# Performance work log

Hardware: AMD Instinct MI355X
Metric: run time of the kernel (lower is better)

Reference implementation:

```python
import jax, jax.numpy as jnp
import numpy as np

B, S, H = 2, 4096, 256
NH, NKV = 8, 4
HD = H // NH          # 32
GROUPS = NH // NKV    # 2
ROPE_BASE = 10000.0


def _rope_cos_sin(seq_len, dim, dtype):
    inv_freq = 1.0 / (ROPE_BASE ** (jnp.arange(0, dim, 2, dtype=jnp.float32) / dim))
    t = jnp.arange(seq_len, dtype=jnp.float32)
    freqs = jnp.outer(t, inv_freq)            # [S, dim/2]
    emb = jnp.concatenate([freqs, freqs], -1)  # [S, dim]
    return jnp.cos(emb).astype(dtype), jnp.sin(emb).astype(dtype)


def _rotate_half(x):
    x1, x2 = jnp.split(x, 2, axis=-1)
    return jnp.concatenate([-x2, x1], axis=-1)


def setup_inputs() -> dict:
    key = jax.random.key(0)
    k0, k1, k2, k3, k4 = jax.random.split(key, 5)
    return {
        "hidden_states": jax.random.normal(k0, (B, S, H), jnp.float32),
        "Wq": jax.random.normal(k1, (H, H), jnp.float32) * 0.02,
        "Wk": jax.random.normal(k2, (NKV * HD, H), jnp.float32) * 0.02,
        "Wv": jax.random.normal(k3, (NKV * HD, H), jnp.float32) * 0.02,
        "Wo": jax.random.normal(k4, (H, H), jnp.float32) * 0.02,
    }


def reference(hidden_states, Wq, Wk, Wv, Wo):
    b, s, _ = hidden_states.shape
    # projections (nn.Linear: x @ W.T)
    q = (hidden_states @ Wq.T).reshape(b, s, NH, HD).transpose(0, 2, 1, 3)   # [b,nh,s,hd]
    k = (hidden_states @ Wk.T).reshape(b, s, NKV, HD).transpose(0, 2, 1, 3)  # [b,nkv,s,hd]
    v = (hidden_states @ Wv.T).reshape(b, s, NKV, HD).transpose(0, 2, 1, 3)
    # RoPE
    cos, sin = _rope_cos_sin(s, HD, hidden_states.dtype)  # [s,hd]
    q = q * cos + _rotate_half(q) * sin
    k = k * cos + _rotate_half(k) * sin
    # GQA: repeat kv heads (repeat_interleave over head dim)
    k = jnp.repeat(k, GROUPS, axis=1)  # [b,nh,s,hd]
    v = jnp.repeat(v, GROUPS, axis=1)
    # scores + causal mask
    scores = jnp.einsum('bhqd,bhkd->bhqk', q, k) / jnp.sqrt(jnp.float32(HD)).astype(q.dtype)
    causal = jnp.triu(jnp.full((s, s), -jnp.inf, dtype=scores.dtype), k=1)
    scores = scores + causal
    attn = jax.nn.softmax(scores.astype(jnp.float32), axis=-1).astype(q.dtype)
    out = jnp.einsum('bhqk,bhkd->bhqd', attn, v)          # [b,nh,s,hd]
    out = out.transpose(0, 2, 1, 3).reshape(b, s, NH * HD)
    return out @ Wo.T
```

## Files before the change

kernel.cpp:

```cpp
#include <hip/hip_runtime.h>
#include <hip/hip_bf16.h>
#include <stdint.h>

#define NB 2
#define SEQ 4096
#define HID 256
#define NHEAD 8
#define NKVH 4
#define HDIM 32

typedef __bf16 bf16;
typedef __bf16 bf16x8 __attribute__((ext_vector_type(8)));
typedef float f32x4 __attribute__((ext_vector_type(4)));

static __device__ __forceinline__ uint16_t bfbits(float f) {
    bf16 h = (bf16)f;
    return __builtin_bit_cast(uint16_t, h);
}
static __device__ __forceinline__ uint32_t pack_bf16(float lo, float hi) {
    return (uint32_t)bfbits(lo) | ((uint32_t)bfbits(hi) << 16);
}
static __device__ __forceinline__ float fexp2(float x) {
#if __has_builtin(__builtin_amdgcn_exp2f)
    return __builtin_amdgcn_exp2f(x);
#else
    float r; asm("v_exp_f32 %0, %1" : "=v"(r) : "v"(x)); return r;
#endif
}
static __device__ __forceinline__ void gld_lds16(const void* g, void* l) {
    __builtin_amdgcn_global_load_lds(
        (const __attribute__((address_space(1))) void*)g,
        (__attribute__((address_space(3))) void*)l, 16, 0, 0);
}

__global__ __launch_bounds__(256) void qkv_proj(
    const float* __restrict__ hs, const float* __restrict__ Wq,
    const float* __restrict__ Wk, const float* __restrict__ Wv,
    bf16* __restrict__ qws, bf16* __restrict__ kws, bf16* __restrict__ vtws)
{
    __shared__ bf16 As[64][136];
    __shared__ bf16 Bs[64][136];
    const int t = threadIdx.x;
    const int wid = t >> 6, lane = t & 63;
    const int g = lane >> 4, c = lane & 15;
    const int n0 = blockIdx.x * 64;
    const int m0 = blockIdx.y * 64;

    const float* bsrc; int ro;
    if (n0 < 256)      { bsrc = Wq; ro = n0; }
    else if (n0 < 384) { bsrc = Wk; ro = n0 - 256; }
    else               { bsrc = Wv; ro = n0 - 384; }

    const f32x4 zf = {0.f, 0.f, 0.f, 0.f};
    f32x4 acc[4] = {zf, zf, zf, zf};

    const int c4 = t & 31;
    const int rb = t >> 5;

    for (int ks = 0; ks < 256; ks += 128) {
        __syncthreads();
        #pragma unroll
        for (int i = 0; i < 8; ++i) {
            int row = i * 8 + rb;
            float4 v = *(const float4*)&hs[(size_t)(m0 + row) * HID + ks + c4 * 4];
            ushort4 w; w.x = bfbits(v.x); w.y = bfbits(v.y); w.z = bfbits(v.z); w.w = bfbits(v.w);
            *(ushort4*)&As[row][c4 * 4] = w;
        }
        #pragma unroll
        for (int i = 0; i < 8; ++i) {
            int row = i * 8 + rb;
            float4 v = *(const float4*)&bsrc[(size_t)(ro + row) * HID + ks + c4 * 4];
            ushort4 w; w.x = bfbits(v.x); w.y = bfbits(v.y); w.z = bfbits(v.z); w.w = bfbits(v.w);
            *(ushort4*)&Bs[row][c4 * 4] = w;
        }
        __syncthreads();
        #pragma unroll
        for (int kk = 0; kk < 128; kk += 32) {
            bf16x8 af = *(const bf16x8*)&As[wid * 16 + c][kk + g * 8];
            #pragma unroll
            for (int nt = 0; nt < 4; ++nt) {
                bf16x8 bfr = *(const bf16x8*)&Bs[nt * 16 + c][kk + g * 8];
                acc[nt] = __builtin_amdgcn_mfma_f32_16x16x32_bf16(af, bfr, acc[nt], 0, 0, 0);
            }
        }
    }

    const float qscale = 1.4426950408889634f * 0.17677669529663687f;
    const float invf = exp2f(-0.83048202372184f * (float)c);
    #pragma unroll
    for (int r = 0; r < 4; ++r) {
        int m = m0 + wid * 16 + g * 4 + r;
        int b = m >> 12, s = m & (SEQ - 1);
        float sn, cs;
        sincosf((float)s * invf, &sn, &cs);
        if (n0 < 256) {
            #pragma unroll
            for (int np = 0; np < 4; np += 2) {
                int h = (n0 + np * 16) >> 5;
                float x1 = acc[np][r], x2 = acc[np + 1][r];
                float y1 = (x1 * cs - x2 * sn) * qscale;
                float y2 = (x2 * cs + x1 * sn) * qscale;
                size_t base = ((size_t)(b * NHEAD + h) * SEQ + s) * HDIM;
                qws[base + c] = (bf16)y1;
                qws[base + 16 + c] = (bf16)y2;
            }
        } else if (n0 < 384) {
            #pragma unroll
            for (int np = 0; np < 4; np += 2) {
                int kh = (n0 - 256 + np * 16) >> 5;
                float x1 = acc[np][r], x2 = acc[np + 1][r];
                float y1 = x1 * cs - x2 * sn;
                float y2 = x2 * cs + x1 * sn;
                size_t base = ((size_t)(b * NKVH + kh) * SEQ + s) * HDIM;
                kws[base + c] = (bf16)y1;
                kws[base + 16 + c] = (bf16)y2;
            }
        } else {
            #pragma unroll
            for (int nt = 0; nt < 4; ++nt) {
                int ng = n0 + nt * 16 + c - 384;
                int vh = ng >> 5, d = ng & 31;
                vtws[((size_t)(b * NKVH + vh) * HDIM + d) * SEQ + s] = (bf16)acc[nt][r];
            }
        }
    }
}

__global__ __launch_bounds__(256, 2) void attn_fwd(
    const bf16* __restrict__ qws, const bf16* __restrict__ kws,
    const bf16* __restrict__ vtws, bf16* __restrict__ att)
{
    __shared__ bf16 Kb[2][128 * 32];
    __shared__ bf16 Vb[2][32 * 128];
    __shared__ float tr[4][16 * 33];
    const int t = threadIdx.x;
    const int w = t >> 6, lane = t & 63;
    const int g = lane >> 4, c = lane & 15;
    const int wg = blockIdx.x;
    const int h = wg & 7;
    const int rem = (wg >> 3) & 31;
    const int b = rem & 1;
    const int tp = rem >> 1;
    const int T = (wg < 256) ? (31 - tp) : tp;
    const int kvh = h >> 1;
    const bf16* Kg = kws + (size_t)(b * NKVH + kvh) * SEQ * HDIM;
    const bf16* Vg = vtws + (size_t)(b * NKVH + kvh) * HDIM * SEQ;
    const int nsteps = T + 1;
    const int q0 = T * 128 + w * 32;

    const bf16* Qb = qws + (size_t)(b * NHEAD + h) * SEQ * HDIM;
    bf16x8 qf0 = *(const bf16x8*)&Qb[(size_t)(q0 + c) * HDIM + g * 8];
    bf16x8 qf1 = *(const bf16x8*)&Qb[(size_t)(q0 + 16 + c) * HDIM + g * 8];

    const bf16* kg_t = Kg + t * 8;
    const int seg_s = (t & 8) | ((t & 7) ^ ((t >> 4) & 7));
    const bf16* vg_tA = Vg + (size_t)(t >> 4) * SEQ + seg_s * 8;
    const bf16* vg_tB = vg_tA + (size_t)16 * SEQ;
    char* kl = (char*)&Kb[0][0] + w * 1024;
    char* vl = (char*)&Vb[0][0] + w * 1024;

    const int kperm = 8 * (c >> 2) + (c & 3);
    const int kro = kperm * 64 + g * 16;
    const int cx = c & 7;
    const int vrow0 = c * 256;
    const int voff0 = ((g) ^ cx) << 4;
    const int voff1 = ((4 + g) ^ cx) << 4;
    const int voff2 = 128 + voff0;
    const int voff3 = 128 + voff1;

    const f32x4 zf = {0.f, 0.f, 0.f, 0.f};
    union { uint32_t u[4]; bf16x8 v; } onesf;
    onesf.u[0] = onesf.u[1] = onesf.u[2] = onesf.u[3] = 0x3F803F80u;

    f32x4 o00 = zf, o01 = zf, ol0 = zf;
    f32x4 o10 = zf, o11 = zf, ol1 = zf;

    gld_lds16(kg_t, kl);
    gld_lds16(kg_t + 2048, kl + 4096);
    gld_lds16(vg_tA, vl);
    gld_lds16(vg_tB, vl + 4096);
    __syncthreads();

    #pragma unroll 1
    for (int s = 0; s < nsteps; ++s) {
        const int sn = s + 1;
        if (sn < nsteps) {
            const int bo = (sn & 1) * 8192;
            gld_lds16(kg_t + (size_t)sn * 4096, kl + bo);
            gld_lds16(kg_t + (size_t)sn * 4096 + 2048, kl + bo + 4096);
            gld_lds16(vg_tA + (size_t)sn * 128, vl + bo);
            gld_lds16(vg_tB + (size_t)sn * 128, vl + bo + 4096);
        }
        const char* kbuf = (const char*)&Kb[s & 1][0];
        const char* vbuf = (const char*)&Vb[s & 1][0];
        const bool diag = (s == T);
        const int qo0 = w * 32 + c;
        #pragma unroll
        for (int j = 0; j < 4; ++j) {
            if (diag && j > w) continue;
            const int voffj = (j == 0) ? voff0 : (j == 1) ? voff1 : (j == 2) ? voff2 : voff3;
            bf16x8 kf0 = *(const bf16x8*)(kbuf + j * 2048 + kro);
            bf16x8 kf1 = *(const bf16x8*)(kbuf + j * 2048 + kro + 256);
            bf16x8 vfA = *(const bf16x8*)(vbuf + vrow0 + voffj);
            bf16x8 vfB = *(const bf16x8*)(vbuf + 4096 + vrow0 + voffj);
            {
                f32x4 st0 = __builtin_amdgcn_mfma_f32_16x16x32_bf16(kf0, qf0, zf, 0, 0, 0);
                f32x4 st1 = __builtin_amdgcn_mfma_f32_16x16x32_bf16(kf1, qf0, zf, 0, 0, 0);
                if (diag) {
                    #pragma unroll
                    for (int r = 0; r < 4; ++r) {
                        if (j * 32 + 8 * g + r > qo0)     st0[r] = -1e30f;
                        if (j * 32 + 8 * g + 4 + r > qo0) st1[r] = -1e30f;
                    }
                }
                float p0 = fexp2(st0[0]), p1 = fexp2(st0[1]), p2 = fexp2(st0[2]), p3 = fexp2(st0[3]);
                float p4 = fexp2(st1[0]), p5 = fexp2(st1[1]), p6 = fexp2(st1[2]), p7 = fexp2(st1[3]);
                union { uint32_t u[4]; bf16x8 v; } pb;
                asm("v_cvt_pk_bf16_f32 %0, %1, %2" : "=v"(pb.u[0]) : "v"(p0), "v"(p1));
                asm("v_cvt_pk_bf16_f32 %0, %1, %2" : "=v"(pb.u[1]) : "v"(p2), "v"(p3));
                asm("v_cvt_pk_bf16_f32 %0, %1, %2" : "=v"(pb.u[2]) : "v"(p4), "v"(p5));
                asm("v_cvt_pk_bf16_f32 %0, %1, %2" : "=v"(pb.u[3]) : "v"(p6), "v"(p7));
                o00 = __builtin_amdgcn_mfma_f32_16x16x32_bf16(vfA, pb.v, o00, 0, 0, 0);
                o01 = __builtin_amdgcn_mfma_f32_16x16x32_bf16(vfB, pb.v, o01, 0, 0, 0);
                ol0 = __builtin_amdgcn_mfma_f32_16x16x32_bf16(onesf.v, pb.v, ol0, 0, 0, 0);
            }
            {
                f32x4 st0 = __builtin_amdgcn_mfma_f32_16x16x32_bf16(kf0, qf1, zf, 0, 0, 0);
                f32x4 st1 = __builtin_amdgcn_mfma_f32_16x16x32_bf16(kf1, qf1, zf, 0, 0, 0);
                if (diag) {
                    const int qo1 = qo0 + 16;
                    #pragma unroll
                    for (int r = 0; r < 4; ++r) {
                        if (j * 32 + 8 * g + r > qo1)     st0[r] = -1e30f;
                        if (j * 32 + 8 * g + 4 + r > qo1) st1[r] = -1e30f;
                    }
                }
                float p0 = fexp2(st0[0]), p1 = fexp2(st0[1]), p2 = fexp2(st0[2]), p3 = fexp2(st0[3]);
                float p4 = fexp2(st1[0]), p5 = fexp2(st1[1]), p6 = fexp2(st1[2]), p7 = fexp2(st1[3]);
                union { uint32_t u[4]; bf16x8 v; } pb;
                asm("v_cvt_pk_bf16_f32 %0, %1, %2" : "=v"(pb.u[0]) : "v"(p0), "v"(p1));
                asm("v_cvt_pk_bf16_f32 %0, %1, %2" : "=v"(pb.u[1]) : "v"(p2), "v"(p3));
                asm("v_cvt_pk_bf16_f32 %0, %1, %2" : "=v"(pb.u[2]) : "v"(p4), "v"(p5));
                asm("v_cvt_pk_bf16_f32 %0, %1, %2" : "=v"(pb.u[3]) : "v"(p6), "v"(p7));
                o10 = __builtin_amdgcn_mfma_f32_16x16x32_bf16(vfA, pb.v, o10, 0, 0, 0);
                o11 = __builtin_amdgcn_mfma_f32_16x16x32_bf16(vfB, pb.v, o11, 0, 0, 0);
                ol1 = __builtin_amdgcn_mfma_f32_16x16x32_bf16(onesf.v, pb.v, ol1, 0, 0, 0);
            }
        }
        __syncthreads();
    }

    #pragma unroll 1
    for (int j = 0; j < 2; ++j) {
        f32x4 a0 = j ? o10 : o00;
        f32x4 a1 = j ? o11 : o01;
        f32x4 al = j ? ol1 : ol0;
        float inv = 1.0f / al[0];
        #pragma unroll
        for (int r = 0; r < 4; ++r) {
            tr[w][c * 33 + 4 * g + r]      = a0[r] * inv;
            tr[w][c * 33 + 16 + 4 * g + r] = a1[r] * inv;
        }
        int q = lane >> 2, dp = (lane & 3) * 8;
        uint32_t u0 = pack_bf16(tr[w][q * 33 + dp + 0], tr[w][q * 33 + dp + 1]);
        uint32_t u1 = pack_bf16(tr[w][q * 33 + dp + 2], tr[w][q * 33 + dp + 3]);
        uint32_t u2 = pack_bf16(tr[w][q * 33 + dp + 4], tr[w][q * 33 + dp + 5]);
        uint32_t u3 = pack_bf16(tr[w][q * 33 + dp + 6], tr[w][q * 33 + dp + 7]);
        size_t base = ((size_t)b * SEQ + q0 + j * 16 + q) * HID + h * HDIM + dp;
        *(uint4*)&att[base] = make_uint4(u0, u1, u2, u3);
    }
}

__global__ __launch_bounds__(256) void out_proj(
    const bf16* __restrict__ att, const float* __restrict__ Wo,
    float* __restrict__ out)
{
    __shared__ bf16 As[64][136];
    __shared__ bf16 Bs[64][136];
    const int t = threadIdx.x;
    const int wid = t >> 6, lane = t & 63;
    const int g = lane >> 4, c = lane & 15;
    const int n0 = blockIdx.x * 64;
    const int m0 = blockIdx.y * 64;

    const f32x4 zf = {0.f, 0.f, 0.f, 0.f};
    f32x4 acc[4] = {zf, zf, zf, zf};

    const int c4 = t & 31;
    const int rb = t >> 5;

    for (int ks = 0; ks < 256; ks += 128) {
        __syncthreads();
        #pragma unroll
        for (int i = 0; i < 8; ++i) {
            int row = i * 8 + rb;
            ushort4 v = *(const ushort4*)&att[(size_t)(m0 + row) * HID + ks + c4 * 4];
            *(ushort4*)&As[row][c4 * 4] = v;
        }
        #pragma unroll
        for (int i = 0; i < 8; ++i) {
            int row = i * 8 + rb;
            float4 v = *(const float4*)&Wo[(size_t)(n0 + row) * HID + ks + c4 * 4];
            ushort4 w; w.x = bfbits(v.x); w.y = bfbits(v.y); w.z = bfbits(v.z); w.w = bfbits(v.w);
            *(ushort4*)&Bs[row][c4 * 4] = w;
        }
        __syncthreads();
        #pragma unroll
        for (int kk = 0; kk < 128; kk += 32) {
            bf16x8 af = *(const bf16x8*)&As[wid * 16 + c][kk + g * 8];
            #pragma unroll
            for (int nt = 0; nt < 4; ++nt) {
                bf16x8 bfr = *(const bf16x8*)&Bs[nt * 16 + c][kk + g * 8];
                acc[nt] = __builtin_amdgcn_mfma_f32_16x16x32_bf16(af, bfr, acc[nt], 0, 0, 0);
            }
        }
    }

    #pragma unroll
    for (int nt = 0; nt < 4; ++nt) {
        #pragma unroll
        for (int r = 0; r < 4; ++r) {
            int m = m0 + wid * 16 + g * 4 + r;
            out[(size_t)m * HID + n0 + nt * 16 + c] = acc[nt][r];
        }
    }
}

extern "C" void kernel_launch(void* const* d_in, const int* in_sizes, int n_in,
                              void* d_out, int out_size, void* d_ws, size_t ws_size,
                              hipStream_t stream) {
    const float* hs = (const float*)d_in[0];
    const float* Wq = (const float*)d_in[1];
    const float* Wk = (const float*)d_in[2];
    const float* Wv = (const float*)d_in[3];
    const float* Wo = (const float*)d_in[4];
    char* ws = (char*)d_ws;
    bf16* qws  = (bf16*)(ws);
    bf16* kws  = (bf16*)(ws + 4194304);
    bf16* vtws = (bf16*)(ws + 6291456);
    bf16* att  = (bf16*)(ws + 8388608);

    qkv_proj<<<dim3(8, 128), 256, 0, stream>>>(hs, Wq, Wk, Wv, qws, kws, vtws);
    attn_fwd<<<512, 256, 0, stream>>>(qws, kws, vtws, att);
    out_proj<<<dim3(4, 128), 256, 0, stream>>>(att, Wo, (float*)d_out);
}
```

Measured before the change: 72.96 us.

## Halve attention query tile to 64 rows and double grid with higher occupancy

The attention kernel now processes 64 query rows per workgroup (16 per wave) with 64-key K/V tiles instead of 128, launching 1024 workgroups and requesting 4 workgroups per CU. Tiles are issued longest-first rather than by the previous pairing of long and short tiles. The aim is better load balance and latency hiding through more resident waves and smaller LDS use. In exchange, each K/V tile is reused by fewer queries, so global and LDS traffic per unit of work roughly doubles, and each wave does half as much independent MFMA work per iteration.

```diff
diff --git a/kernel.cpp b/kernel.cpp
--- a/kernel.cpp
+++ b/kernel.cpp
@@ -126,147 +126,132 @@
     }
 }
 
-__global__ __launch_bounds__(256, 2) void attn_fwd(
+__global__ __launch_bounds__(256, 4) void attn_fwd(
     const bf16* __restrict__ qws, const bf16* __restrict__ kws,
     const bf16* __restrict__ vtws, bf16* __restrict__ att)
 {
-    __shared__ bf16 Kb[2][128 * 32];
-    __shared__ bf16 Vb[2][32 * 128];
+    __shared__ bf16 Kb[2][64 * 32];
+    __shared__ bf16 Vb[2][32 * 64];
     __shared__ float tr[4][16 * 33];
     const int t = threadIdx.x;
     const int w = t >> 6, lane = t & 63;
     const int g = lane >> 4, c = lane & 15;
     const int wg = blockIdx.x;
     const int h = wg & 7;
-    const int rem = (wg >> 3) & 31;
-    const int b = rem & 1;
-    const int tp = rem >> 1;
-    const int T = (wg < 256) ? (31 - tp) : tp;
+    const int rest = wg >> 3;
+    const int b = rest & 1;
+    const int TT = 63 - (rest >> 1);
     const int kvh = h >> 1;
     const bf16* Kg = kws + (size_t)(b * NKVH + kvh) * SEQ * HDIM;
     const bf16* Vg = vtws + (size_t)(b * NKVH + kvh) * HDIM * SEQ;
-    const int nsteps = T + 1;
-    const int q0 = T * 128 + w * 32;
+    const int nsteps = TT + 1;
+    const int q0 = TT * 64 + w * 16;
 
     const bf16* Qb = qws + (size_t)(b * NHEAD + h) * SEQ * HDIM;
-    bf16x8 qf0 = *(const bf16x8*)&Qb[(size_t)(q0 + c) * HDIM + g * 8];
-    bf16x8 qf1 = *(const bf16x8*)&Qb[(size_t)(q0 + 16 + c) * HDIM + g * 8];
-
+    bf16x8 qf = *(const bf16x8*)&Qb[(size_t)(q0 + c) * HDIM + g * 8];
+
+    const int sd = t >> 3, sseg = t & 7;
     const bf16* kg_t = Kg + t * 8;
-    const int seg_s = (t & 8) | ((t & 7) ^ ((t >> 4) & 7));
-    const bf16* vg_tA = Vg + (size_t)(t >> 4) * SEQ + seg_s * 8;
-    const bf16* vg_tB = vg_tA + (size_t)16 * SEQ;
+    const bf16* vg_t = Vg + (size_t)sd * SEQ + (sseg ^ (sd & 7)) * 8;
     char* kl = (char*)&Kb[0][0] + w * 1024;
     char* vl = (char*)&Vb[0][0] + w * 1024;
 
     const int kperm = 8 * (c >> 2) + (c & 3);
     const int kro = kperm * 64 + g * 16;
     const int cx = c & 7;
-    const int vrow0 = c * 256;
-    const int voff0 = ((g) ^ cx) << 4;
-    const int voff1 = ((4 + g) ^ cx) << 4;
-    const int voff2 = 128 + voff0;
-    const int voff3 = 128 + voff1;
+    const int vro0 = c * 128, vro1 = (16 + c) * 128;
+    const int voffA = ((g) ^ cx) << 4;
+    const int voffB = (((4 + g)) ^ cx) << 4;
 
     const f32x4 zf = {0.f, 0.f, 0.f, 0.f};
     union { uint32_t u[4]; bf16x8 v; } onesf;
     onesf.u[0] = onesf.u[1] = onesf.u[2] = onesf.u[3] = 0x3F803F80u;
 
-    f32x4 o00 = zf, o01 = zf, ol0 = zf;
-    f32x4 o10 = zf, o11 = zf, ol1 = zf;
+    f32x4 o0 = zf, o1 = zf, ol = zf;
 
     gld_lds16(kg_t, kl);
-    gld_lds16(kg_t + 2048, kl + 4096);
-    gld_lds16(vg_tA, vl);
-    gld_lds16(vg_tB, vl + 4096);
+    gld_lds16(vg_t, vl);
     __syncthreads();
 
     #pragma unroll 1
     for (int s = 0; s < nsteps; ++s) {
         const int sn = s + 1;
         if (sn < nsteps) {
-            const int bo = (sn & 1) * 8192;
-            gld_lds16(kg_t + (size_t)sn * 4096, kl + bo);
-            gld_lds16(kg_t + (size_t)sn * 4096 + 2048, kl + bo + 4096);
-            gld_lds16(vg_tA + (size_t)sn * 128, vl + bo);
-            gld_lds16(vg_tB + (size_t)sn * 128, vl + bo + 4096);
+            const int bo = (sn & 1) * 4096;
+            gld_lds16(kg_t + (size_t)sn * 2048, kl + bo);
+            gld_lds16(vg_t + (size_t)sn * 64, vl + bo);
         }
         const char* kbuf = (const char*)&Kb[s & 1][0];
         const char* vbuf = (const char*)&Vb[s & 1][0];
-        const bool diag = (s == T);
-        const int qo0 = w * 32 + c;
-        #pragma unroll
-        for (int j = 0; j < 4; ++j) {
-            if (diag && j > w) continue;
-            const int voffj = (j == 0) ? voff0 : (j == 1) ? voff1 : (j == 2) ? voff2 : voff3;
-            bf16x8 kf0 = *(const bf16x8*)(kbuf + j * 2048 + kro);
-            bf16x8 kf1 = *(const bf16x8*)(kbuf + j * 2048 + kro + 256);
-            bf16x8 vfA = *(const bf16x8*)(vbuf + vrow0 + voffj);
-            bf16x8 vfB = *(const bf16x8*)(vbuf + 4096 + vrow0 + voffj);
-            {
-                f32x4 st0 = __builtin_amdgcn_mfma_f32_16x16x32_bf16(kf0, qf0, zf, 0, 0, 0);
-                f32x4 st1 = __builtin_amdgcn_mfma_f32_16x16x32_bf16(kf1, qf0, zf, 0, 0, 0);
-                if (diag) {
-                    #pragma unroll
-                    for (int r = 0; r < 4; ++r) {
-                        if (j * 32 + 8 * g + r > qo0)     st0[r] = -1e30f;
-                        if (j * 32 + 8 * g + 4 + r > qo0) st1[r] = -1e30f;
-                    }
+        const bool diag = (s == TT);
+        const int qoff = w * 16 + c;
+
+        {
+            bf16x8 kf0 = *(const bf16x8*)(kbuf + kro);
+            bf16x8 kf1 = *(const bf16x8*)(kbuf + kro + 256);
+            f32x4 st0 = __builtin_amdgcn_mfma_f32_16x16x32_bf16(kf0, qf, zf, 0, 0, 0);
+            f32x4 st1 = __builtin_amdgcn_mfma_f32_16x16x32_bf16(kf1, qf, zf, 0, 0, 0);
+            if (diag) {
+                #pragma unroll
+                for (int r = 0; r < 4; ++r) {
+                    if (8 * g + r > qoff)     st0[r] = -1e30f;
+                    if (8 * g + 4 + r > qoff) st1[r] = -1e30f;
                 }
-                float p0 = fexp2(st0[0]), p1 = fexp2(st0[1]), p2 = fexp2(st0[2]), p3 = fexp2(st0[3]);
-                float p4 = fexp2(st1[0]), p5 = fexp2(st1[1]), p6 = fexp2(st1[2]), p7 = fexp2(st1[3]);
-                union { uint32_t u[4]; bf16x8 v; } pb;
-                asm("v_cvt_pk_bf16_f32 %0, %1, %2" : "=v"(pb.u[0]) : "v"(p0), "v"(p1));
-                asm("v_cvt_pk_bf16_f32 %0, %1, %2" : "=v"(pb.u[1]) : "v"(p2), "v"(p3));
-                asm("v_cvt_pk_bf16_f32 %0, %1, %2" : "=v"(pb.u[2]) : "v"(p4), "v"(p5));
-                asm("v_cvt_pk_bf16_f32 %0, %1, %2" : "=v"(pb.u[3]) : "v"(p6), "v"(p7));
-                o00 = __builtin_amdgcn_mfma_f32_16x16x32_bf16(vfA, pb.v, o00, 0, 0, 0);
-                o01 = __builtin_amdgcn_mfma_f32_16x16x32_bf16(vfB, pb.v, o01, 0, 0, 0);
-                ol0 = __builtin_amdgcn_mfma_f32_16x16x32_bf16(onesf.v, pb.v, ol0, 0, 0, 0);
-            }
-            {
-                f32x4 st0 = __builtin_amdgcn_mfma_f32_16x16x32_bf16(kf0, qf1, zf, 0, 0, 0);
-                f32x4 st1 = __builtin_amdgcn_mfma_f32_16x16x32_bf16(kf1, qf1, zf, 0, 0, 0);
-                if (diag) {
-                    const int qo1 = qo0 + 16;
-                    #pragma unroll
-                    for (int r = 0; r < 4; ++r) {
-                        if (j * 32 + 8 * g + r > qo1)     st0[r] = -1e30f;
-                        if (j * 32 + 8 * g + 4 + r > qo1) st1[r] = -1e30f;
-                    }
+            }
+            float p0 = fexp2(st0[0]), p1 = fexp2(st0[1]), p2 = fexp2(st0[2]), p3 = fexp2(st0[3]);
+            float p4 = fexp2(st1[0]), p5 = fexp2(st1[1]), p6 = fexp2(st1[2]), p7 = fexp2(st1[3]);
+            union { uint32_t u[4]; bf16x8 v; } pb;
+            asm("v_cvt_pk_bf16_f32 %0, %1, %2" : "=v"(pb.u[0]) : "v"(p0), "v"(p1));
+            asm("v_cvt_pk_bf16_f32 %0, %1, %2" : "=v"(pb.u[1]) : "v"(p2), "v"(p3));
+            asm("v_cvt_pk_bf16_f32 %0, %1, %2" : "=v"(pb.u[2]) : "v"(p4), "v"(p5));
+            asm("v_cvt_pk_bf16_f32 %0, %1, %2" : "=v"(pb.u[3]) : "v"(p6), "v"(p7));
+            bf16x8 vfA = *(const bf16x8*)(vbuf + vro0 + voffA);
+            bf16x8 vfB = *(const bf16x8*)(vbuf + vro1 + voffA);
+            o0 = __builtin_amdgcn_mfma_f32_16x16x32_bf16(vfA, pb.v, o0, 0, 0, 0);
+            o1 = __builtin_amdgcn_mfma_f32_16x16x32_bf16(vfB, pb.v, o1, 0, 0, 0);
+            ol = __builtin_amdgcn_mfma_f32_16x16x32_bf16(onesf.v, pb.v, ol, 0, 0, 0);
+        }
+        if (!diag || w >= 2) {
+            bf16x8 kf2 = *(const bf16x8*)(kbuf + kro + 2048);
+            bf16x8 kf3 = *(const bf16x8*)(kbuf + kro + 2304);
+            f32x4 st2 = __builtin_amdgcn_mfma_f32_16x16x32_bf16(kf2, qf, zf, 0, 0, 0);
+            f32x4 st3 = __builtin_amdgcn_mfma_f32_16x16x32_bf16(kf3, qf, zf, 0, 0, 0);
+            if (diag) {
+                #pragma unroll
+                for (int r = 0; r < 4; ++r) {
+                    if (32 + 8 * g + r > qoff)     st2[r] = -1e30f;
+                    if (32 + 8 * g + 4 + r > qoff) st3[r] = -1e30f;
                 }
-                float p0 = fexp2(st0[0]), p1 = fexp2(st0[1]), p2 = fexp2(st0[2]), p3 = fexp2(st0[3]);
-                float p4 = fexp2(st1[0]), p5 = fexp2(st1[1]), p6 = fexp2(st1[2]), p7 = fexp2(st1[3]);
-                union { uint32_t u[4]; bf16x8 v; } pb;
-                asm("v_cvt_pk_bf16_f32 %0, %1, %2" : "=v"(pb.u[0]) : "v"(p0), "v"(p1));
-                asm("v_cvt_pk_bf16_f32 %0, %1, %2" : "=v"(pb.u[1]) : "v"(p2), "v"(p3));
-                asm("v_cvt_pk_bf16_f32 %0, %1, %2" : "=v"(pb.u[2]) : "v"(p4), "v"(p5));
-                asm("v_cvt_pk_bf16_f32 %0, %1, %2" : "=v"(pb.u[3]) : "v"(p6), "v"(p7));
-                o10 = __builtin_amdgcn_mfma_f32_16x16x32_bf16(vfA, pb.v, o10, 0, 0, 0);
-                o11 = __builtin_amdgcn_mfma_f32_16x16x32_bf16(vfB, pb.v, o11, 0, 0, 0);
-                ol1 = __builtin_amdgcn_mfma_f32_16x16x32_bf16(onesf.v, pb.v, ol1, 0, 0, 0);
-            }
-        }
-        __syncthreads();
-    }
-
-    #pragma unroll 1
-    for (int j = 0; j < 2; ++j) {
-        f32x4 a0 = j ? o10 : o00;
-        f32x4 a1 = j ? o11 : o01;
-        f32x4 al = j ? ol1 : ol0;
-        float inv = 1.0f / al[0];
+            }
+            float p0 = fexp2(st2[0]), p1 = fexp2(st2[1]), p2 = fexp2(st2[2]), p3 = fexp2(st2[3]);
+            float p4 = fexp2(st3[0]), p5 = fexp2(st3[1]), p6 = fexp2(st3[2]), p7 = fexp2(st3[3]);
+            union { uint32_t u[4]; bf16x8 v; } pb;
+            asm("v_cvt_pk_bf16_f32 %0, %1, %2" : "=v"(pb.u[0]) : "v"(p0), "v"(p1));
+            asm("v_cvt_pk_bf16_f32 %0, %1, %2" : "=v"(pb.u[1]) : "v"(p2), "v"(p3));
+            asm("v_cvt_pk_bf16_f32 %0, %1, %2" : "=v"(pb.u[2]) : "v"(p4), "v"(p5));
+            asm("v_cvt_pk_bf16_f32 %0, %1, %2" : "=v"(pb.u[3]) : "v"(p6), "v"(p7));
+            bf16x8 vfA = *(const bf16x8*)(vbuf + vro0 + voffB);
+            bf16x8 vfB = *(const bf16x8*)(vbuf + vro1 + voffB);
+            o0 = __builtin_amdgcn_mfma_f32_16x16x32_bf16(vfA, pb.v, o0, 0, 0, 0);
+            o1 = __builtin_amdgcn_mfma_f32_16x16x32_bf16(vfB, pb.v, o1, 0, 0, 0);
+            ol = __builtin_amdgcn_mfma_f32_16x16x32_bf16(onesf.v, pb.v, ol, 0, 0, 0);
+        }
+        __syncthreads();
+    }
+
+    {
+        float inv = 1.0f / ol[0];
         #pragma unroll
         for (int r = 0; r < 4; ++r) {
-            tr[w][c * 33 + 4 * g + r]      = a0[r] * inv;
-            tr[w][c * 33 + 16 + 4 * g + r] = a1[r] * inv;
+            tr[w][c * 33 + 4 * g + r]      = o0[r] * inv;
+            tr[w][c * 33 + 16 + 4 * g + r] = o1[r] * inv;
         }
         int q = lane >> 2, dp = (lane & 3) * 8;
         uint32_t u0 = pack_bf16(tr[w][q * 33 + dp + 0], tr[w][q * 33 + dp + 1]);
         uint32_t u1 = pack_bf16(tr[w][q * 33 + dp + 2], tr[w][q * 33 + dp + 3]);
         uint32_t u2 = pack_bf16(tr[w][q * 33 + dp + 4], tr[w][q * 33 + dp + 5]);
         uint32_t u3 = pack_bf16(tr[w][q * 33 + dp + 6], tr[w][q * 33 + dp + 7]);
-        size_t base = ((size_t)b * SEQ + q0 + j * 16 + q) * HID + h * HDIM + dp;
+        size_t base = ((size_t)b * SEQ + q0 + q) * HID + h * HDIM + dp;
         *(uint4*)&att[base] = make_uint4(u0, u1, u2, u3);
     }
 }
@@ -341,6 +326,6 @@
     bf16* att  = (bf16*)(ws + 8388608);
 
     qkv_proj<<<dim3(8, 128), 256, 0, stream>>>(hs, Wq, Wk, Wv, qws, kws, vtws);
-    attn_fwd<<<512, 256, 0, stream>>>(qws, kws, vtws, att);
+    attn_fwd<<<1024, 256, 0, stream>>>(qws, kws, vtws, att);
     out_proj<<<dim3(4, 128), 256, 0, stream>>>(att, Wo, (float*)d_out);
 }
```

After: 72.43 us. No clear change (-0.7%).

## Halve attention query tile to 64 rows with 2-wave blocks and 1024 workgroups

Applied to the files above, without the earlier changes.

Restructures the attention kernel to use 64-query, 64-key tiles processed by 2 wavefronts per block instead of 128-query tiles with 4 waves, doubling the grid to 1024 blocks. The LDS layout, V swizzle, and loads are adjusted to the smaller tile, and the diagonal masking is specialised so wave 0 skips the second key half. The descending-work ordering replaces the previous paired long/short tile scheduling. This aims at finer load balancing and higher occupancy, but it doubles K/V reloads per query and adds more per-step barrier overhead.

```diff
diff --git a/kernel.cpp b/kernel.cpp
--- a/kernel.cpp
+++ b/kernel.cpp
@@ -126,35 +126,35 @@
     }
 }
 
-__global__ __launch_bounds__(256, 2) void attn_fwd(
+__global__ __launch_bounds__(128, 4) void attn_fwd(
     const bf16* __restrict__ qws, const bf16* __restrict__ kws,
     const bf16* __restrict__ vtws, bf16* __restrict__ att)
 {
-    __shared__ bf16 Kb[2][128 * 32];
-    __shared__ bf16 Vb[2][32 * 128];
-    __shared__ float tr[4][16 * 33];
+    __shared__ bf16 Kb[2][64 * 32];
+    __shared__ bf16 Vb[2][32 * 64];
+    __shared__ float tr[2][16 * 33];
     const int t = threadIdx.x;
     const int w = t >> 6, lane = t & 63;
     const int g = lane >> 4, c = lane & 15;
     const int wg = blockIdx.x;
     const int h = wg & 7;
-    const int rem = (wg >> 3) & 31;
-    const int b = rem & 1;
-    const int tp = rem >> 1;
-    const int T = (wg < 256) ? (31 - tp) : tp;
+    const int rest = wg >> 3;
+    const int b = rest & 1;
+    const int TT = 63 - (rest >> 1);
     const int kvh = h >> 1;
     const bf16* Kg = kws + (size_t)(b * NKVH + kvh) * SEQ * HDIM;
     const bf16* Vg = vtws + (size_t)(b * NKVH + kvh) * HDIM * SEQ;
-    const int nsteps = T + 1;
-    const int q0 = T * 128 + w * 32;
+    const int nsteps = TT + 1;
+    const int q0 = TT * 64 + w * 32;
 
     const bf16* Qb = qws + (size_t)(b * NHEAD + h) * SEQ * HDIM;
     bf16x8 qf0 = *(const bf16x8*)&Qb[(size_t)(q0 + c) * HDIM + g * 8];
     bf16x8 qf1 = *(const bf16x8*)&Qb[(size_t)(q0 + 16 + c) * HDIM + g * 8];
 
+    const int sd = t >> 3, sseg = t & 7;
     const bf16* kg_t = Kg + t * 8;
-    const int seg_s = (t & 8) | ((t & 7) ^ ((t >> 4) & 7));
-    const bf16* vg_tA = Vg + (size_t)(t >> 4) * SEQ + seg_s * 8;
+    const int seg_s = sseg ^ (sd & 7);
+    const bf16* vg_tA = Vg + (size_t)sd * SEQ + seg_s * 8;
     const bf16* vg_tB = vg_tA + (size_t)16 * SEQ;
     char* kl = (char*)&Kb[0][0] + w * 1024;
     char* vl = (char*)&Vb[0][0] + w * 1024;
@@ -162,11 +162,9 @@
     const int kperm = 8 * (c >> 2) + (c & 3);
     const int kro = kperm * 64 + g * 16;
     const int cx = c & 7;
-    const int vrow0 = c * 256;
-    const int voff0 = ((g) ^ cx) << 4;
-    const int voff1 = ((4 + g) ^ cx) << 4;
-    const int voff2 = 128 + voff0;
-    const int voff3 = 128 + voff1;
+    const int vro0 = c * 128, vro1 = (16 + c) * 128;
+    const int voffA = ((g) ^ cx) << 4;
+    const int voffB = ((4 + g) ^ cx) << 4;
 
     const f32x4 zf = {0.f, 0.f, 0.f, 0.f};
     union { uint32_t u[4]; bf16x8 v; } onesf;
@@ -176,41 +174,39 @@
     f32x4 o10 = zf, o11 = zf, ol1 = zf;
 
     gld_lds16(kg_t, kl);
-    gld_lds16(kg_t + 2048, kl + 4096);
+    gld_lds16(kg_t + 1024, kl + 2048);
     gld_lds16(vg_tA, vl);
-    gld_lds16(vg_tB, vl + 4096);
+    gld_lds16(vg_tB, vl + 2048);
     __syncthreads();
 
     #pragma unroll 1
     for (int s = 0; s < nsteps; ++s) {
         const int sn = s + 1;
         if (sn < nsteps) {
-            const int bo = (sn & 1) * 8192;
-            gld_lds16(kg_t + (size_t)sn * 4096, kl + bo);
-            gld_lds16(kg_t + (size_t)sn * 4096 + 2048, kl + bo + 4096);
-            gld_lds16(vg_tA + (size_t)sn * 128, vl + bo);
-            gld_lds16(vg_tB + (size_t)sn * 128, vl + bo + 4096);
+            const int bo = (sn & 1) * 4096;
+            gld_lds16(kg_t + (size_t)sn * 2048, kl + bo);
+            gld_lds16(kg_t + (size_t)sn * 2048 + 1024, kl + bo + 2048);
+            gld_lds16(vg_tA + (size_t)sn * 64, vl + bo);
+            gld_lds16(vg_tB + (size_t)sn * 64, vl + bo + 2048);
         }
         const char* kbuf = (const char*)&Kb[s & 1][0];
         const char* vbuf = (const char*)&Vb[s & 1][0];
-        const bool diag = (s == T);
+        const bool diag = (s == TT);
         const int qo0 = w * 32 + c;
-        #pragma unroll
-        for (int j = 0; j < 4; ++j) {
-            if (diag && j > w) continue;
-            const int voffj = (j == 0) ? voff0 : (j == 1) ? voff1 : (j == 2) ? voff2 : voff3;
-            bf16x8 kf0 = *(const bf16x8*)(kbuf + j * 2048 + kro);
-            bf16x8 kf1 = *(const bf16x8*)(kbuf + j * 2048 + kro + 256);
-            bf16x8 vfA = *(const bf16x8*)(vbuf + vrow0 + voffj);
-            bf16x8 vfB = *(const bf16x8*)(vbuf + 4096 + vrow0 + voffj);
+
+        {
+            bf16x8 kf0 = *(const bf16x8*)(kbuf + kro);
+            bf16x8 kf1 = *(const bf16x8*)(kbuf + kro + 256);
+            bf16x8 vfA0 = *(const bf16x8*)(vbuf + vro0 + voffA);
+            bf16x8 vfA1 = *(const bf16x8*)(vbuf + vro1 + voffA);
             {
                 f32x4 st0 = __builtin_amdgcn_mfma_f32_16x16x32_bf16(kf0, qf0, zf, 0, 0, 0);
                 f32x4 st1 = __builtin_amdgcn_mfma_f32_16x16x32_bf16(kf1, qf0, zf, 0, 0, 0);
                 if (diag) {
                     #pragma unroll
                     for (int r = 0; r < 4; ++r) {
-                        if (j * 32 + 8 * g + r > qo0)     st0[r] = -1e30f;
-                        if (j * 32 + 8 * g + 4 + r > qo0) st1[r] = -1e30f;
+                        if (8 * g + r > qo0)     st0[r] = -1e30f;
+                        if (8 * g + 4 + r > qo0) st1[r] = -1e30f;
                     }
                 }
                 float p0 = fexp2(st0[0]), p1 = fexp2(st0[1]), p2 = fexp2(st0[2]), p3 = fexp2(st0[3]);
@@ -220,8 +216,8 @@
                 asm("v_cvt_pk_bf16_f32 %0, %1, %2" : "=v"(pb.u[1]) : "v"(p2), "v"(p3));
                 asm("v_cvt_pk_bf16_f32 %0, %1, %2" : "=v"(pb.u[2]) : "v"(p4), "v"(p5));
                 asm("v_cvt_pk_bf16_f32 %0, %1, %2" : "=v"(pb.u[3]) : "v"(p6), "v"(p7));
-                o00 = __builtin_amdgcn_mfma_f32_16x16x32_bf16(vfA, pb.v, o00, 0, 0, 0);
-                o01 = __builtin_amdgcn_mfma_f32_16x16x32_bf16(vfB, pb.v, o01, 0, 0, 0);
+                o00 = __builtin_amdgcn_mfma_f32_16x16x32_bf16(vfA0, pb.v, o00, 0, 0, 0);
+                o01 = __builtin_amdgcn_mfma_f32_16x16x32_bf16(vfA1, pb.v, o01, 0, 0, 0);
                 ol0 = __builtin_amdgcn_mfma_f32_16x16x32_bf16(onesf.v, pb.v, ol0, 0, 0, 0);
             }
             {
@@ -231,8 +227,8 @@
                     const int qo1 = qo0 + 16;
                     #pragma unroll
                     for (int r = 0; r < 4; ++r) {
-                        if (j * 32 + 8 * g + r > qo1)     st0[r] = -1e30f;
-                        if (j * 32 + 8 * g + 4 + r > qo1) st1[r] = -1e30f;
+                        if (8 * g + r > qo1)     st0[r] = -1e30f;
+                        if (8 * g + 4 + r > qo1) st1[r] = -1e30f;
                     }
                 }
                 float p0 = fexp2(st0[0]), p1 = fexp2(st0[1]), p2 = fexp2(st0[2]), p3 = fexp2(st0[3]);
@@ -242,8 +238,57 @@
                 asm("v_cvt_pk_bf16_f32 %0, %1, %2" : "=v"(pb.u[1]) : "v"(p2), "v"(p3));
                 asm("v_cvt_pk_bf16_f32 %0, %1, %2" : "=v"(pb.u[2]) : "v"(p4), "v"(p5));
                 asm("v_cvt_pk_bf16_f32 %0, %1, %2" : "=v"(pb.u[3]) : "v"(p6), "v"(p7));
-                o10 = __builtin_amdgcn_mfma_f32_16x16x32_bf16(vfA, pb.v, o10, 0, 0, 0);
-                o11 = __builtin_amdgcn_mfma_f32_16x16x32_bf16(vfB, pb.v, o11, 0, 0, 0);
+                o10 = __builtin_amdgcn_mfma_f32_16x16x32_bf16(vfA0, pb.v, o10, 0, 0, 0);
+                o11 = __builtin_amdgcn_mfma_f32_16x16x32_bf16(vfA1, pb.v, o11, 0, 0, 0);
+                ol1 = __builtin_amdgcn_mfma_f32_16x16x32_bf16(onesf.v, pb.v, ol1, 0, 0, 0);
+            }
+        }
+        if (!diag || w == 1) {
+            bf16x8 kf2 = *(const bf16x8*)(kbuf + kro + 2048);
+            bf16x8 kf3 = *(const bf16x8*)(kbuf + kro + 2304);
+            bf16x8 vfB0 = *(const bf16x8*)(vbuf + vro0 + voffB);
+            bf16x8 vfB1 = *(const bf16x8*)(vbuf + vro1 + voffB);
+            {
+                f32x4 st2 = __builtin_amdgcn_mfma_f32_16x16x32_bf16(kf2, qf0, zf, 0, 0, 0);
+                f32x4 st3 = __builtin_amdgcn_mfma_f32_16x16x32_bf16(kf3, qf0, zf, 0, 0, 0);
+                if (diag) {
+                    #pragma unroll
+                    for (int r = 0; r < 4; ++r) {
+                        if (32 + 8 * g + r > qo0)     st2[r] = -1e30f;
+                        if (32 + 8 * g + 4 + r > qo0) st3[r] = -1e30f;
+                    }
+                }
+                float p0 = fexp2(st2[0]), p1 = fexp2(st2[1]), p2 = fexp2(st2[2]), p3 = fexp2(st2[3]);
+                float p4 = fexp2(st3[0]), p5 = fexp2(st3[1]), p6 = fexp2(st3[2]), p7 = fexp2(st3[3]);
+                union { uint32_t u[4]; bf16x8 v; } pb;
+                asm("v_cvt_pk_bf16_f32 %0, %1, %2" : "=v"(pb.u[0]) : "v"(p0), "v"(p1));
+                asm("v_cvt_pk_bf16_f32 %0, %1, %2" : "=v"(pb.u[1]) : "v"(p2), "v"(p3));
+                asm("v_cvt_pk_bf16_f32 %0, %1, %2" : "=v"(pb.u[2]) : "v"(p4), "v"(p5));
+                asm("v_cvt_pk_bf16_f32 %0, %1, %2" : "=v"(pb.u[3]) : "v"(p6), "v"(p7));
+                o00 = __builtin_amdgcn_mfma_f32_16x16x32_bf16(vfB0, pb.v, o00, 0, 0, 0);
+                o01 = __builtin_amdgcn_mfma_f32_16x16x32_bf16(vfB1, pb.v, o01, 0, 0, 0);
+                ol0 = __builtin_amdgcn_mfma_f32_16x16x32_bf16(onesf.v, pb.v, ol0, 0, 0, 0);
+            }
+            {
+                f32x4 st2 = __builtin_amdgcn_mfma_f32_16x16x32_bf16(kf2, qf1, zf, 0, 0, 0);
+                f32x4 st3 = __builtin_amdgcn_mfma_f32_16x16x32_bf16(kf3, qf1, zf, 0, 0, 0);
+                if (diag) {
+                    const int qo1 = qo0 + 16;
+                    #pragma unroll
+                    for (int r = 0; r < 4; ++r) {
+                        if (32 + 8 * g + r > qo1)     st2[r] = -1e30f;
+                        if (32 + 8 * g + 4 + r > qo1) st3[r] = -1e30f;
+                    }
+                }
+                float p0 = fexp2(st2[0]), p1 = fexp2(st2[1]), p2 = fexp2(st2[2]), p3 = fexp2(st2[3]);
+                float p4 = fexp2(st3[0]), p5 = fexp2(st3[1]), p6 = fexp2(st3[2]), p7 = fexp2(st3[3]);
+                union { uint32_t u[4]; bf16x8 v; } pb;
+                asm("v_cvt_pk_bf16_f32 %0, %1, %2" : "=v"(pb.u[0]) : "v"(p0), "v"(p1));
+                asm("v_cvt_pk_bf16_f32 %0, %1, %2" : "=v"(pb.u[1]) : "v"(p2), "v"(p3));
+                asm("v_cvt_pk_bf16_f32 %0, %1, %2" : "=v"(pb.u[2]) : "v"(p4), "v"(p5));
+                asm("v_cvt_pk_bf16_f32 %0, %1, %2" : "=v"(pb.u[3]) : "v"(p6), "v"(p7));
+                o10 = __builtin_amdgcn_mfma_f32_16x16x32_bf16(vfB0, pb.v, o10, 0, 0, 0);
+                o11 = __builtin_amdgcn_mfma_f32_16x16x32_bf16(vfB1, pb.v, o11, 0, 0, 0);
                 ol1 = __builtin_amdgcn_mfma_f32_16x16x32_bf16(onesf.v, pb.v, ol1, 0, 0, 0);
             }
         }
@@ -341,6 +386,6 @@
     bf16* att  = (bf16*)(ws + 8388608);
 
     qkv_proj<<<dim3(8, 128), 256, 0, stream>>>(hs, Wq, Wk, Wv, qws, kws, vtws);
-    attn_fwd<<<512, 256, 0, stream>>>(qws, kws, vtws, att);
+    attn_fwd<<<1024, 128, 0, stream>>>(qws, kws, vtws, att);
     out_proj<<<dim3(4, 128), 256, 0, stream>>>(att, Wo, (float*)d_out);
 }
```

New measurement: 81.69 us. +12.0%, slower.
